# Optimization experiments

Measured on AMD Instinct MI355X. Metric: run time of the kernel, lower is better.

The kernel has to match this reference:

```python
import jax, jax.numpy as jnp
import numpy as np

B, L, D = 1, 4096, 1152
N, H = 16, 72            # num_heads, head_dim = d_model // num_heads
S = 64                   # num_patches_side = image_size // patch_size = 896 // 14
BASE = 100.0             # base_frequency for 2D RoPE
EPS = 1e-6


def _rmsnorm(t, scale):
    # t: [..., H]; Gemma-style zero-init scale -> multiply by (1 + scale)
    var = jnp.mean(t * t, axis=-1, keepdims=True)
    t = t * jax.lax.rsqrt(var + EPS)
    if scale is not None:
        t = t * (1.0 + scale)
    return t


def _rope_axis(t, pos):
    # t: [B, L, N, half]; pos: [B, L]. Split-half rotation with given base.
    half = t.shape[-1]
    freqs = BASE ** (-jnp.arange(0, half, 2, dtype=jnp.float32) * 2.0 / half)  # [half//2]
    ang = pos[:, :, None] * freqs                      # [B, L, half//2]
    cos = jnp.cos(ang)[:, :, None, :]
    sin = jnp.sin(ang)[:, :, None, :]
    t1, t2 = t[..., : half // 2], t[..., half // 2 :]
    return jnp.concatenate([t1 * cos - t2 * sin, t1 * sin + t2 * cos], axis=-1)


def _rope_2d(t, rows, cols):
    # first half of head_dim rotated by row position, second half by column position
    h2 = t.shape[-1] // 2
    return jnp.concatenate(
        [_rope_axis(t[..., :h2], rows), _rope_axis(t[..., h2:], cols)], axis=-1
    )


def setup_inputs() -> dict:
    key = jax.random.key(0)
    ks = jax.random.split(key, 5)
    s = 0.02
    return {
        "x": jax.random.normal(ks[0], (B, L, D), dtype=jnp.float32),
        "q_w": jax.random.normal(ks[1], (D, D), dtype=jnp.float32) * s,
        "q_b": jnp.zeros((D,), dtype=jnp.float32),
        "kv_w": jax.random.normal(ks[2], (D, 2 * D), dtype=jnp.float32) * s,
        "kv_b": jnp.zeros((2 * D,), dtype=jnp.float32),
        "o_w": jax.random.normal(ks[3], (D, D), dtype=jnp.float32) * s,
        "o_b": jnp.zeros((D,), dtype=jnp.float32),
        "q_scale": jnp.zeros((H,), dtype=jnp.float32),  # RMSNorm zero_init
        "k_scale": jnp.zeros((H,), dtype=jnp.float32),  # RMSNorm zero_init
    }


def reference(x, q_w, q_b, kv_w, kv_b, o_w, o_b, q_scale, k_scale):
    q = (x @ q_w + q_b).reshape(B, L, N, H)
    kv = (x @ kv_w + kv_b).reshape(B, L, 2, N, H)
    k, v = kv[:, :, 0], kv[:, :, 1]

    q = _rmsnorm(q, q_scale)
    k = _rmsnorm(k, k_scale)
    v = _rmsnorm(v, None)  # with_scale=False

    rows = jnp.repeat(jnp.arange(S, dtype=jnp.float32), S)[None, :L]  # [1, L]
    cols = jnp.tile(jnp.arange(S, dtype=jnp.float32), S)[None, :L]
    rows = jnp.broadcast_to(rows, (B, L))
    cols = jnp.broadcast_to(cols, (B, L))

    q = _rope_2d(q, rows, cols)  # scale = 1.0
    k = _rope_2d(k, rows, cols)

    attn = jnp.einsum("bqnh,bknh->bnqk", q, k)          # [B, N, L, L]
    attn = jax.nn.softmax(attn, axis=-1)
    out = jnp.einsum("bnqk,bknh->bqnh", attn, v).reshape(B, L, D)
    return out @ o_w + o_b
```

## Files before the change

### kernel.cpp

```cpp
#include <hip/hip_runtime.h>
#include <cstdint>
#include <cstddef>

#define LSEQ 4096
#define DMODEL 1152
#define NH 16
#define HD 72
#define HP96 96
#define HP80 80
#define NQKV 3456

typedef unsigned short u16;
typedef unsigned int u32;
typedef __attribute__((ext_vector_type(4))) float f32x4;
typedef __attribute__((ext_vector_type(4))) u32 u32x4;
typedef _Float16 f16x8 __attribute__((ext_vector_type(8), may_alias));
typedef unsigned short us8 __attribute__((ext_vector_type(8), may_alias));
typedef unsigned short us4 __attribute__((ext_vector_type(4), may_alias));

static __device__ __forceinline__ u16 f2h(float f) {
  _Float16 h = (_Float16)f;
  return __builtin_bit_cast(u16, h);
}
static __device__ __forceinline__ float h2f(u16 b) {
  return (float)__builtin_bit_cast(_Float16, b);
}

__global__ void k_cvt_f16(const float* __restrict__ src, u16* __restrict__ dst, int n4) {
  int i = blockIdx.x * blockDim.x + threadIdx.x;
  int stride = gridDim.x * blockDim.x;
  for (; i < n4; i += stride) {
    float4 v = ((const float4*)src)[i];
    us4 o; o[0] = f2h(v.x); o[1] = f2h(v.y); o[2] = f2h(v.z); o[3] = f2h(v.w);
    ((us4*)dst)[i] = o;
  }
}

__global__ void k_transp_w(const float* __restrict__ src, u16* __restrict__ dst, int K, int N) {
  __shared__ float tile[32][33];
  int tx = threadIdx.x & 31, ty = threadIdx.x >> 5;
  int n0 = blockIdx.x * 32, k0 = blockIdx.y * 32;
#pragma unroll
  for (int j = 0; j < 4; ++j)
    tile[ty + j * 8][tx] = src[(size_t)(k0 + ty + j * 8) * N + n0 + tx];
  __syncthreads();
#pragma unroll
  for (int j = 0; j < 4; ++j)
    dst[(size_t)(n0 + ty + j * 8) * K + k0 + tx] = f2h(tile[tx][ty + j * 8]);
}

template <bool OUTF32>
__global__ __launch_bounds__(256) void k_gemm_bt(
    const u16* __restrict__ A, const u16* __restrict__ Bt,
    const float* __restrict__ bias, void* __restrict__ Cout,
    int M, int N, int K) {
  __shared__ __align__(16) u16 sA[128][40];
  __shared__ __align__(16) u16 sB[128][40];
  int t = threadIdx.x;
  int l = t & 63, w = t >> 6, lo = l & 15, hi = l >> 4;
  int m0 = blockIdx.y * 128, n0 = blockIdx.x * 128;
  int wm = (w >> 1) * 64, wn = (w & 1) * 64;
  int sr = t >> 1, sh = (t & 1) * 16;
  const u16* pa = A + (size_t)(m0 + sr) * K + sh;
  const u16* pb = Bt + (size_t)(n0 + sr) * K + sh;
  f32x4 acc[4][4] = {};
  us8 ra0 = *(const us8*)(pa), ra1 = *(const us8*)(pa + 8);
  us8 rb0 = *(const us8*)(pb), rb1 = *(const us8*)(pb + 8);
  int nk = K >> 5;
  for (int ks = 0; ks < nk; ++ks) {
    __syncthreads();
    *(us8*)&sA[sr][sh] = ra0; *(us8*)&sA[sr][sh + 8] = ra1;
    *(us8*)&sB[sr][sh] = rb0; *(us8*)&sB[sr][sh + 8] = rb1;
    if (ks + 1 < nk) {
      int off = (ks + 1) * 32;
      ra0 = *(const us8*)(pa + off); ra1 = *(const us8*)(pa + off + 8);
      rb0 = *(const us8*)(pb + off); rb1 = *(const us8*)(pb + off + 8);
    }
    __syncthreads();
    f16x8 af[4], bf[4];
#pragma unroll
    for (int mi = 0; mi < 4; ++mi) af[mi] = *(const f16x8*)&sA[wm + mi * 16 + lo][hi * 8];
#pragma unroll
    for (int ni = 0; ni < 4; ++ni) bf[ni] = *(const f16x8*)&sB[wn + ni * 16 + lo][hi * 8];
#pragma unroll
    for (int mi = 0; mi < 4; ++mi)
#pragma unroll
      for (int ni = 0; ni < 4; ++ni)
        acc[mi][ni] = __builtin_amdgcn_mfma_f32_16x16x32_f16(af[mi], bf[ni], acc[mi][ni], 0, 0, 0);
  }
#pragma unroll
  for (int mi = 0; mi < 4; ++mi)
#pragma unroll
    for (int ni = 0; ni < 4; ++ni) {
      int row = m0 + wm + mi * 16 + hi * 4;
      int col = n0 + wn + ni * 16 + lo;
      float bv = bias ? bias[col] : 0.0f;
#pragma unroll
      for (int rr = 0; rr < 4; ++rr) {
        float v = acc[mi][ni][rr] + bv;
        if (OUTF32) ((float*)Cout)[(size_t)(row + rr) * N + col] = v;
        else        ((u16*)Cout)[(size_t)(row + rr) * N + col] = f2h(v);
      }
    }
}

__global__ __launch_bounds__(256) void k_norm_rope(
    const u16* __restrict__ qkv,
    const float* __restrict__ q_b, const float* __restrict__ kv_b,
    const float* __restrict__ q_s, const float* __restrict__ k_s,
    u16* __restrict__ qp, u16* __restrict__ kp, u16* __restrict__ vn) {
  __shared__ float s_q[DMODEL], s_k[DMODEL], s_v[DMODEL];
  __shared__ float cs[4][18];
  int t = threadIdx.x;
  int tok = blockIdx.x;
  if (t < 36) {
    int i = t < 18 ? t : t - 18;
    float f = exp2f(-(float)i * (6.6438561897747247f / 9.0f));
    float pos = (t < 18) ? (float)(tok >> 6) : (float)(tok & 63);
    float s, c;
    sincosf(pos * f, &s, &c);
    if (t < 18) { cs[0][i] = c; cs[1][i] = s; }
    else        { cs[2][i] = c; cs[3][i] = s; }
  }
  const u16* rowp = qkv + (size_t)tok * NQKV;
  for (int idx = t; idx < DMODEL; idx += 256) {
    s_q[idx] = h2f(rowp[idx]) + q_b[idx];
    s_k[idx] = h2f(rowp[DMODEL + idx]) + kv_b[idx];
    s_v[idx] = h2f(rowp[2 * DMODEL + idx]) + kv_b[DMODEL + idx];
  }
  __syncthreads();
  int h = t >> 4, sub = t & 15;
  int base = h * HD;
  float aq = 0, ak = 0, av = 0;
#pragma unroll
  for (int j = 0; j < 5; ++j) {
    int idx = sub + 16 * j;
    if (idx < HD) {
      float a = s_q[base + idx], b = s_k[base + idx], c = s_v[base + idx];
      aq += a * a; ak += b * b; av += c * c;
    }
  }
#pragma unroll
  for (int m = 1; m <= 8; m <<= 1) {
    aq += __shfl_xor(aq, m, 64);
    ak += __shfl_xor(ak, m, 64);
    av += __shfl_xor(av, m, 64);
  }
  float rq = rsqrtf(aq / 72.f + 1e-6f);
  float rk = rsqrtf(ak / 72.f + 1e-6f);
  float rv = rsqrtf(av / 72.f + 1e-6f);
  size_t ob96 = ((size_t)h * LSEQ + tok) * HP96;
  size_t ob80 = ((size_t)h * LSEQ + tok) * HP80;
#pragma unroll
  for (int j = 0; j < 6; ++j) {
    int idx = sub + 16 * j;
    float oq = 0.f, ok = 0.f;
    if (idx < HD) {
      int sec = idx >= 36;
      int loc = idx - sec * 36;
      int i = loc >= 18 ? loc - 18 : loc;
      float c = cs[sec * 2 + 0][i], s = cs[sec * 2 + 1][i];
      int p1 = sec * 36 + i, p2 = p1 + 18;
      float q1 = s_q[base + p1] * rq * (1.f + q_s[p1]);
      float q2 = s_q[base + p2] * rq * (1.f + q_s[p2]);
      float k1 = s_k[base + p1] * rk * (1.f + k_s[p1]);
      float k2 = s_k[base + p2] * rk * (1.f + k_s[p2]);
      if (loc < 18) { oq = q1 * c - q2 * s; ok = k1 * c - k2 * s; }
      else          { oq = q1 * s + q2 * c; ok = k1 * s + k2 * c; }
    }
    qp[ob96 + idx] = f2h(oq);
    kp[ob96 + idx] = f2h(ok);
  }
#pragma unroll
  for (int j = 0; j < 5; ++j) {
    int idx = sub + 16 * j;
    float ov = (idx < HD) ? s_v[base + idx] * rv : (idx == 72 ? 1.0f : 0.f);
    vn[ob80 + idx] = f2h(ov);
  }
}

__global__ __launch_bounds__(256) void k_vfrag(const u16* __restrict__ vn, u16* __restrict__ vf) {
  __shared__ u16 tl[32][84];
  int head = blockIdx.y, kb = blockIdx.x;
  int t = threadIdx.x;
  const u16* src = vn + ((size_t)head * LSEQ + kb * 32) * HP80;
  for (int p = t; p < 32 * 20; p += 256) {
    int rr = p / 20, c4 = p % 20;
    *(us4*)&tl[rr][c4 * 4] = *(const us4*)(src + rr * HP80 + c4 * 4);
  }
  __syncthreads();
  u16* dst = vf + ((size_t)head * 128 + kb) * 2560;
  for (int u = t; u < 320; u += 256) {
    int ht = u >> 6, ll = u & 63, lo2 = ll & 15, hi2 = ll >> 4;
    us8 o;
#pragma unroll
    for (int j = 0; j < 8; ++j)
      o[j] = tl[(j >> 2) * 16 + hi2 * 4 + (j & 3)][ht * 16 + lo2];
    *(us8*)&dst[(size_t)u * 8] = o;
  }
}

__global__ __launch_bounds__(256, 2) void k_flash(
    const u16* __restrict__ qp, const u16* __restrict__ kp,
    const u16* __restrict__ vf, u16* __restrict__ attb) {
  __shared__ __align__(16) u16 sK[64][104];
  int t = threadIdx.x;
  int l = t & 63, w = t >> 6, lo = l & 15, hi = l >> 4;
  int id = blockIdx.x, r = id >> 3;
  int qb = r & 31, head = ((r >> 5) << 3) + (id & 7);
  const float L2E = 1.4426950408889634f;

  const u16* qbase = qp + ((size_t)head * LSEQ + qb * 128 + w * 32 + lo) * HP96 + hi * 8;
  f16x8 qf[2][3];
#pragma unroll
  for (int g = 0; g < 2; ++g)
#pragma unroll
    for (int c = 0; c < 3; ++c)
      qf[g][c] = *(const f16x8*)(qbase + g * 16 * HP96 + c * 32);

  f32x4 oacc[2][5] = {};
  float mrun[2];
#pragma unroll
  for (int g = 0; g < 2; ++g) mrun[g] = -__builtin_inff();

  int sr_ = t >> 2, sq4 = (t & 3) * 24;
  const u16* kptr = kp + ((size_t)head * LSEQ + sr_) * HP96 + sq4;
  us8 kx0 = *(const us8*)(kptr), kx1 = *(const us8*)(kptr + 8), kx2 = *(const us8*)(kptr + 16);

  const u16* vptr = vf + (size_t)head * 128 * 2560 + (size_t)l * 8;
  us8 vA[5], vB[5];
#pragma unroll
  for (int ht = 0; ht < 5; ++ht) vA[ht] = *(const us8*)(vptr + ht * 512);
  vptr += 2560;

  for (int kt = 0; kt < 64; ++kt) {
    __syncthreads();
    *(us8*)&sK[sr_][sq4] = kx0; *(us8*)&sK[sr_][sq4 + 8] = kx1; *(us8*)&sK[sr_][sq4 + 16] = kx2;
    if (kt < 63) {
      kx0 = *(const us8*)(kptr + 6144);
      kx1 = *(const us8*)(kptr + 6144 + 8);
      kx2 = *(const us8*)(kptr + 6144 + 16);
      kptr += 6144;
    }
    __syncthreads();
    f32x4 sacc[2][4] = {};
#pragma unroll
    for (int c = 0; c < 3; ++c)
#pragma unroll
      for (int nt = 0; nt < 4; ++nt) {
        f16x8 bk = *(const f16x8*)&sK[lo + 16 * nt][c * 32 + hi * 8];
#pragma unroll
        for (int g = 0; g < 2; ++g)
          sacc[g][nt] = __builtin_amdgcn_mfma_f32_16x16x32_f16(bk, qf[g][c], sacc[g][nt], 0, 0, 0);
      }
    float mt[2];
#pragma unroll
    for (int g = 0; g < 2; ++g) {
      float m = fmaxf(fmaxf(fmaxf(sacc[g][0][0], sacc[g][0][1]), sacc[g][0][2]), sacc[g][0][3]);
#pragma unroll
      for (int nt = 1; nt < 4; ++nt)
        m = fmaxf(m, fmaxf(fmaxf(fmaxf(sacc[g][nt][0], sacc[g][nt][1]), sacc[g][nt][2]), sacc[g][nt][3]));
      m = fmaxf(m, __shfl_xor(m, 16, 64));
      m = fmaxf(m, __shfl_xor(m, 32, 64));
      mt[g] = m;
    }
    bool need = (mt[0] > mrun[0] + 8.f) | (mt[1] > mrun[1] + 8.f);
    if (__any(need)) {
#pragma unroll
      for (int g = 0; g < 2; ++g) {
        float mn = fmaxf(mrun[g], mt[g]);
        float al = exp2f((mrun[g] - mn) * L2E);
        mrun[g] = mn;
#pragma unroll
        for (int ht = 0; ht < 5; ++ht)
#pragma unroll
          for (int rr = 0; rr < 4; ++rr) oacc[g][ht][rr] *= al;
      }
    }
#pragma unroll
    for (int kc = 0; kc < 2; ++kc) {
#pragma unroll
      for (int ht = 0; ht < 5; ++ht) vB[ht] = *(const us8*)(vptr + ht * 512);
      vptr += 2560;
#pragma unroll
      for (int g = 0; g < 2; ++g) {
        float nm = -mrun[g] * L2E;
        float p0[4], p1[4];
#pragma unroll
        for (int rr = 0; rr < 4; ++rr) {
          p0[rr] = exp2f(__builtin_fmaf(sacc[g][2 * kc][rr], L2E, nm));
          p1[rr] = exp2f(__builtin_fmaf(sacc[g][2 * kc + 1][rr], L2E, nm));
        }
        u32x4 pw = {__builtin_bit_cast(u32, __builtin_amdgcn_cvt_pkrtz(p0[0], p0[1])),
                    __builtin_bit_cast(u32, __builtin_amdgcn_cvt_pkrtz(p0[2], p0[3])),
                    __builtin_bit_cast(u32, __builtin_amdgcn_cvt_pkrtz(p1[0], p1[1])),
                    __builtin_bit_cast(u32, __builtin_amdgcn_cvt_pkrtz(p1[2], p1[3]))};
        f16x8 pb = __builtin_bit_cast(f16x8, pw);
#pragma unroll
        for (int ht = 0; ht < 5; ++ht)
          oacc[g][ht] = __builtin_amdgcn_mfma_f32_16x16x32_f16(
              __builtin_bit_cast(f16x8, vA[ht]), pb, oacc[g][ht], 0, 0, 0);
      }
#pragma unroll
      for (int ht = 0; ht < 5; ++ht) vA[ht] = vB[ht];
    }
  }
#pragma unroll
  for (int g = 0; g < 2; ++g) {
    float den = __shfl(oacc[g][4][0], lo + 32, 64);
    float inv = 1.f / den;
    int row = qb * 128 + w * 32 + g * 16 + lo;
    u16* orow = attb + (size_t)row * DMODEL + head * HD;
#pragma unroll
    for (int ht = 0; ht < 5; ++ht)
#pragma unroll
      for (int rr = 0; rr < 4; ++rr) {
        int h = 16 * ht + 4 * hi + rr;
        if (h < HD) orow[h] = f2h(oacc[g][ht][rr] * inv);
      }
  }
}

extern "C" void kernel_launch(void* const* d_in, const int* in_sizes, int n_in,
                              void* d_out, int out_size, void* d_ws, size_t ws_size,
                              hipStream_t stream) {
  const float* x    = (const float*)d_in[0];
  const float* q_w  = (const float*)d_in[1];
  const float* q_b  = (const float*)d_in[2];
  const float* kv_w = (const float*)d_in[3];
  const float* kv_b = (const float*)d_in[4];
  const float* o_w  = (const float*)d_in[5];
  const float* o_b  = (const float*)d_in[6];
  const float* q_s  = (const float*)d_in[7];
  const float* k_s  = (const float*)d_in[8];
  char* ws = (char*)d_ws;
  u16* xb   = (u16*)(ws + 0);
  u16* wT   = (u16*)(ws + 9437184);
  u16* oT   = (u16*)(ws + 17399808);
  u16* qkvb = (u16*)(ws + 20054016);
  u16* qp   = (u16*)(ws + 48365568);
  u16* kp   = (u16*)(ws + 60948480);
  u16* vn   = (u16*)(ws + 73531392);
  u16* vfb  = (u16*)(ws + 0);
  u16* attb = (u16*)(ws + 20054016);

  k_cvt_f16<<<2048, 256, 0, stream>>>(x, xb, LSEQ * DMODEL / 4);
  k_transp_w<<<dim3(36, 36), 256, 0, stream>>>(q_w, wT, DMODEL, DMODEL);
  k_transp_w<<<dim3(72, 36), 256, 0, stream>>>(kv_w, wT + (size_t)DMODEL * DMODEL, DMODEL, 2 * DMODEL);
  k_transp_w<<<dim3(36, 36), 256, 0, stream>>>(o_w, oT, DMODEL, DMODEL);
  k_gemm_bt<false><<<dim3(27, 32), 256, 0, stream>>>(xb, wT, nullptr, qkvb, LSEQ, NQKV, DMODEL);
  k_norm_rope<<<LSEQ, 256, 0, stream>>>(qkvb, q_b, kv_b, q_s, k_s, qp, kp, vn);
  k_vfrag<<<dim3(128, 16), 256, 0, stream>>>(vn, vfb);
  k_flash<<<512, 256, 0, stream>>>(qp, kp, vfb, attb);
  k_gemm_bt<true><<<dim3(9, 32), 256, 0, stream>>>(attb, oT, o_b, (float*)d_out, LSEQ, DMODEL, DMODEL);
}
```

Baseline: 280.3 us.

## Split flash attention along the key sequence and merge the halves in a combine kernel

The flash kernel now splits the key/value range into two halves, launching twice as many blocks. Each block writes a normalized partial output plus its denominator and running max to workspace. A new combine kernel reweights and merges the two partials per token before the output projection. Launch bounds are also raised to 4 blocks per SM to raise occupancy. In exchange it adds extra global traffic for the partial outputs, a second kernel launch, and register pressure from the tighter bound.

```diff
diff --git a/kernel.cpp b/kernel.cpp
--- a/kernel.cpp
+++ b/kernel.cpp
@@ -200,14 +200,14 @@
   }
 }
 
-__global__ __launch_bounds__(256, 2) void k_flash(
+__global__ __launch_bounds__(256, 4) void k_flash(
     const u16* __restrict__ qp, const u16* __restrict__ kp,
-    const u16* __restrict__ vf, u16* __restrict__ attb) {
+    const u16* __restrict__ vf, u16* __restrict__ pbuf, float2* __restrict__ dmb) {
   __shared__ __align__(16) u16 sK[64][104];
   int t = threadIdx.x;
   int l = t & 63, w = t >> 6, lo = l & 15, hi = l >> 4;
   int id = blockIdx.x, r = id >> 3;
-  int qb = r & 31, head = ((r >> 5) << 3) + (id & 7);
+  int half = r & 1, qb = (r >> 1) & 31, head = ((r >> 6) << 3) + (id & 7);
   const float L2E = 1.4426950408889634f;
 
   const u16* qbase = qp + ((size_t)head * LSEQ + qb * 128 + w * 32 + lo) * HP96 + hi * 8;
@@ -224,19 +224,19 @@
   for (int g = 0; g < 2; ++g) mrun[g] = -__builtin_inff();
 
   int sr_ = t >> 2, sq4 = (t & 3) * 24;
-  const u16* kptr = kp + ((size_t)head * LSEQ + sr_) * HP96 + sq4;
+  const u16* kptr = kp + ((size_t)head * LSEQ + half * 2048 + sr_) * HP96 + sq4;
   us8 kx0 = *(const us8*)(kptr), kx1 = *(const us8*)(kptr + 8), kx2 = *(const us8*)(kptr + 16);
 
-  const u16* vptr = vf + (size_t)head * 128 * 2560 + (size_t)l * 8;
+  const u16* vptr = vf + ((size_t)head * 128 + half * 64) * 2560 + (size_t)l * 8;
   us8 vA[5], vB[5];
 #pragma unroll
   for (int ht = 0; ht < 5; ++ht) vA[ht] = *(const us8*)(vptr + ht * 512);
   vptr += 2560;
 
-  for (int kt = 0; kt < 64; ++kt) {
+  for (int kt = 0; kt < 32; ++kt) {
     __syncthreads();
     *(us8*)&sK[sr_][sq4] = kx0; *(us8*)&sK[sr_][sq4 + 8] = kx1; *(us8*)&sK[sr_][sq4 + 16] = kx2;
-    if (kt < 63) {
+    if (kt < 31) {
       kx0 = *(const us8*)(kptr + 6144);
       kx1 = *(const us8*)(kptr + 6144 + 8);
       kx2 = *(const us8*)(kptr + 6144 + 16);
@@ -310,7 +310,7 @@
     float den = __shfl(oacc[g][4][0], lo + 32, 64);
     float inv = 1.f / den;
     int row = qb * 128 + w * 32 + g * 16 + lo;
-    u16* orow = attb + (size_t)row * DMODEL + head * HD;
+    u16* orow = pbuf + ((size_t)half * LSEQ + row) * DMODEL + head * HD;
 #pragma unroll
     for (int ht = 0; ht < 5; ++ht)
 #pragma unroll
@@ -318,6 +318,27 @@
         int h = 16 * ht + 4 * hi + rr;
         if (h < HD) orow[h] = f2h(oacc[g][ht][rr] * inv);
       }
+    if (hi == 0) {
+      float2 dm; dm.x = den; dm.y = mrun[g];
+      dmb[((size_t)half * NH + head) * LSEQ + row] = dm;
+    }
+  }
+}
+
+__global__ __launch_bounds__(384) void k_combine(
+    const u16* __restrict__ pbuf, const float2* __restrict__ dmb, u16* __restrict__ attb) {
+  const float L2E = 1.4426950408889634f;
+  int tok = blockIdx.x, t = threadIdx.x;
+  for (int c = t; c < DMODEL; c += 384) {
+    int head = c / HD;
+    float2 dm0 = dmb[(size_t)head * LSEQ + tok];
+    float2 dm1 = dmb[((size_t)NH + head) * LSEQ + tok];
+    float M = fmaxf(dm0.y, dm1.y);
+    float w0 = dm0.x * exp2f((dm0.y - M) * L2E);
+    float w1 = dm1.x * exp2f((dm1.y - M) * L2E);
+    float o0 = h2f(pbuf[(size_t)tok * DMODEL + c]);
+    float o1 = h2f(pbuf[((size_t)LSEQ + tok) * DMODEL + c]);
+    attb[(size_t)tok * DMODEL + c] = f2h((w0 * o0 + w1 * o1) / (w0 + w1));
   }
 }
 
@@ -342,7 +363,9 @@
   u16* kp   = (u16*)(ws + 60948480);
   u16* vn   = (u16*)(ws + 73531392);
   u16* vfb  = (u16*)(ws + 0);
+  float2* dmb = (float2*)(ws + 10485760);
   u16* attb = (u16*)(ws + 20054016);
+  u16* pbuf = (u16*)(ws + 29491200);
 
   k_cvt_f16<<<2048, 256, 0, stream>>>(x, xb, LSEQ * DMODEL / 4);
   k_transp_w<<<dim3(36, 36), 256, 0, stream>>>(q_w, wT, DMODEL, DMODEL);
@@ -351,6 +374,7 @@
   k_gemm_bt<false><<<dim3(27, 32), 256, 0, stream>>>(xb, wT, nullptr, qkvb, LSEQ, NQKV, DMODEL);
   k_norm_rope<<<LSEQ, 256, 0, stream>>>(qkvb, q_b, kv_b, q_s, k_s, qp, kp, vn);
   k_vfrag<<<dim3(128, 16), 256, 0, stream>>>(vn, vfb);
-  k_flash<<<512, 256, 0, stream>>>(qp, kp, vfb, attb);
+  k_flash<<<1024, 256, 0, stream>>>(qp, kp, vfb, pbuf, dmb);
+  k_combine<<<LSEQ, 384, 0, stream>>>(pbuf, dmb, attb);
   k_gemm_bt<true><<<dim3(9, 32), 256, 0, stream>>>(attb, oT, o_b, (float*)d_out, LSEQ, DMODEL, DMODEL);
 }
```

After: 393.7 us. 40.4% more time.
